# Kernel tuning notes

Measured on AMD Instinct MI355X. Metric: run time of the kernel, lower is better.

The kernel has to match this reference:

```python
import jax, jax.numpy as jnp
import numpy as np

N = 50000   # nodes per graph
E = 500000  # edges per graph
F_IN = 128  # num_features
H = 128     # hidden_channels
C = 64      # num_classes
G = 64      # graphs per batch
NEG_SLOPE = 0.2


def setup_inputs() -> dict:
    key = jax.random.key(0)
    ks = jax.random.split(key, 16)
    s = 1.0 / np.sqrt(H)
    return {
        "x1": jax.random.normal(ks[0], (N, F_IN), jnp.float32),
        "x2": jax.random.normal(ks[1], (N, F_IN), jnp.float32),
        # stacked params for the 2 GATConv layers (F_IN == H so shapes match)
        "convW": jax.random.normal(ks[2], (2, H, H), jnp.float32) * s,
        "att_src": jax.random.normal(ks[3], (2, H), jnp.float32) * s,
        "att_dst": jax.random.normal(ks[4], (2, H), jnp.float32) * s,
        "conv_b": jnp.zeros((2, H), jnp.float32),
        "mlp_w1": jax.random.normal(ks[5], (H, H), jnp.float32) * s,
        "mlp_b1": jnp.zeros((H,), jnp.float32),
        "mlp_w2": jax.random.normal(ks[6], (H, C), jnp.float32) * s,
        "mlp_b2": jnp.zeros((C,), jnp.float32),
        "edge_index1": jax.random.randint(ks[7], (2, E), 0, N, jnp.int64),
        "batch1": jnp.sort(jax.random.randint(ks[8], (N,), 0, G, jnp.int64)),
        "edge_index2": jax.random.randint(ks[9], (2, E), 0, N, jnp.int64),
        "batch2": jnp.sort(jax.random.randint(ks[10], (N,), 0, G, jnp.int64)),
    }


def gat_conv(x, src, dst, W, a_s, a_d, b):
    # PyG GATConv, heads=1, add_self_loops already applied in src/dst
    n = x.shape[0]
    h = x @ W                                   # [N, H]
    alpha_s = h @ a_s                           # [N]
    alpha_d = h @ a_d                           # [N]
    e = alpha_s[src] + alpha_d[dst]             # [Etot]
    e = jnp.where(e > 0, e, NEG_SLOPE * e)      # leaky_relu
    # segment softmax over incoming edges of each dst node
    m = jax.ops.segment_max(e, dst, num_segments=n)
    ex = jnp.exp(e - m[dst])
    denom = jax.ops.segment_sum(ex, dst, num_segments=n)
    alpha = ex / denom[dst]                     # [Etot]
    out = jax.ops.segment_sum(h[src] * alpha[:, None], dst, num_segments=n)
    return out + b


def reference(x1, x2, convW, att_src, att_dst, conv_b,
              mlp_w1, mlp_b1, mlp_w2, mlp_b2,
              edge_index1, batch1, edge_index2, batch2):
    def branch(x, ei):
        n = x.shape[0]
        loops = jnp.arange(n, dtype=ei.dtype)
        src = jnp.concatenate([ei[0], loops])
        dst = jnp.concatenate([ei[1], loops])
        # num_layers=3 -> 2 convs; i != num_layers-1 always true -> ELU after each
        for l in range(2):
            x = gat_conv(x, src, dst, convW[l], att_src[l], att_dst[l], conv_b[l])
            x = jax.nn.elu(x)
            # dropout p=0.5 is identity in eval mode
        return jax.nn.relu(x @ mlp_w1 + mlp_b1) @ mlp_w2 + mlp_b2

    h1 = branch(x1, edge_index1)
    h2 = branch(x2, edge_index2)
    p1 = jax.ops.segment_sum(h1, batch1, num_segments=G)  # [G, C]
    p2 = jax.ops.segment_sum(h2, batch2, num_segments=G)  # [G, C]
    return p1.T @ p2                                      # [C, C]
```

## Files before the change

### kernel.cpp

```cpp
#include <hip/hip_runtime.h>
#include <cstdint>
#include <cstddef>

#define NNODES 50000
#define NEDGES 500000
#define NTOT (NEDGES + NNODES)
#define HDIM 128
#define CDIM 64
#define GDIM 64
#define NB 250
#define NPB 200
#define CHUNK 2048
#define NCHB ((NEDGES + CHUNK - 1) / CHUNK)

typedef __bf16 bf16x8 __attribute__((ext_vector_type(8)));
typedef __bf16 bf16x2 __attribute__((ext_vector_type(2)));
typedef float f32x4 __attribute__((ext_vector_type(4)));


__global__ __launch_bounds__(256) void k_setup(const float* __restrict__ convW,
                                               const float* __restrict__ w1,
                                               const float* __restrict__ w2,
                                               const float* __restrict__ a_s,
                                               const float* __restrict__ a_d,
                                               __bf16* __restrict__ WtC,
                                               __bf16* __restrict__ Wt1,
                                               __bf16* __restrict__ Wt2,
                                               float* __restrict__ Wa,
                                               float* __restrict__ p) {
    int b = blockIdx.x, tid = threadIdx.x;
    if (b < 128) {
        int i = b * 256 + tid;
        int mat = i >> 14, rem = i & 16383;
        int k = rem >> 7, n = rem & 127;
        WtC[mat * 16384 + n * 128 + k] = (__bf16)convW[i];
    } else if (b < 192) {
        int i = (b - 128) * 256 + tid;
        int k = i >> 7, n = i & 127;
        Wt1[n * 128 + k] = (__bf16)w1[i];
    } else if (b < 224) {
        int i = (b - 192) * 256 + tid;
        int k = i >> 6, n = i & 63;
        Wt2[n * 128 + k] = (__bf16)w2[i];
    } else if (b == 224) {
        for (int o = tid; o < 512; o += 256) {
            int l = o >> 8, r = o & 255;
            int type = r >> 7, k = r & 127;
            const float* a = (type ? a_d : a_s) + l * 128;
            const float* Wrow = convW + l * 16384 + k * 128;
            float s = 0.f;
            for (int j = 0; j < 128; j++) s += Wrow[j] * a[j];
            Wa[o] = s;
        }
    } else {
        for (int i = tid; i < 2 * GDIM * CDIM; i += 256) p[i] = 0.f;
    }
}


__global__ __launch_bounds__(256) void k_bhist(const int* __restrict__ ei0,
                                               const int* __restrict__ ei1,
                                               int* __restrict__ bcntB, int e) {
    __shared__ int h[NB];
    const int* dst = (blockIdx.y ? ei1 : ei0) + NEDGES;
    int* bcnt = bcntB + blockIdx.y * NB;
    for (int t = threadIdx.x; t < NB; t += 256) h[t] = 0;
    __syncthreads();
    int base = blockIdx.x * CHUNK;
    int lim = min(base + CHUNK, e);
    for (int i = base + threadIdx.x; i < lim; i += 256) atomicAdd(&h[dst[i] / NPB], 1);
    __syncthreads();
    for (int t = threadIdx.x; t < NB; t += 256)
        if (h[t]) atomicAdd(&bcnt[t], h[t]);
}

__global__ __launch_bounds__(256) void k_bscan(const int* __restrict__ bcntB,
                                               int* __restrict__ boffB,
                                               int* __restrict__ bcurB) {
    __shared__ int s[256];
    int t = threadIdx.x;
    const int* bcnt = bcntB + blockIdx.y * NB;
    int* boff = boffB + blockIdx.y * (NB + 1);
    int* bcur = bcurB + blockIdx.y * NB;
    int v = (t < NB) ? bcnt[t] : 0;
    s[t] = v;
    __syncthreads();
    for (int off = 1; off < 256; off <<= 1) {
        int x = (t >= off) ? s[t - off] : 0;
        __syncthreads();
        s[t] += x;
        __syncthreads();
    }
    if (t < NB) {
        boff[t + 1] = s[t];
        bcur[t] = s[t] - v;
        if (t == 0) boff[0] = 0;
    }
}

__global__ __launch_bounds__(256) void k_part(const int* __restrict__ ei0,
                                              const int* __restrict__ ei1,
                                              int* __restrict__ bcurB,
                                              int2* __restrict__ partB, int e) {
    __shared__ int cnt[NB], boffL[NB], gbase[NB], cur2[NB];
    __shared__ int tmp[256];
    __shared__ int2 staged[CHUNK];
    const int* eis = blockIdx.y ? ei1 : ei0;
    int* bcur = bcurB + blockIdx.y * NB;
    int2* part = partB + blockIdx.y * (size_t)NEDGES;
    int t = threadIdx.x;
    for (int i = t; i < NB; i += 256) { cnt[i] = 0; cur2[i] = 0; }
    __syncthreads();
    int base = blockIdx.x * CHUNK;
    int lim = min(base + CHUNK, e);
    int nloc = lim - base;

    int s_[8], d_[8], b_[8];
    bool v_[8];
#pragma unroll
    for (int k = 0; k < 8; k++) {
        int i = base + k * 256 + t;
        v_[k] = i < lim;
        s_[k] = 0; d_[k] = 0; b_[k] = 0;
        if (v_[k]) {
            s_[k] = eis[i];
            d_[k] = eis[NEDGES + i];
            b_[k] = d_[k] / NPB;
            atomicAdd(&cnt[b_[k]], 1);
        }
    }
    __syncthreads();
    tmp[t] = (t < NB) ? cnt[t] : 0;
    __syncthreads();
    for (int off = 1; off < 256; off <<= 1) {
        int x = (t >= off) ? tmp[t - off] : 0;
        __syncthreads();
        tmp[t] += x;
        __syncthreads();
    }
    if (t < NB) boffL[t] = tmp[t] - cnt[t];
    __syncthreads();
    if (t < NB) {
        int c = cnt[t];
        gbase[t] = c ? atomicAdd(&bcur[t], c) : 0;
    }
    __syncthreads();
#pragma unroll
    for (int k = 0; k < 8; k++) {
        if (v_[k]) {
            int pos = atomicAdd(&cur2[b_[k]], 1);
            staged[boffL[b_[k]] + pos] = make_int2(s_[k], d_[k]);
        }
    }
    __syncthreads();
    for (int i = t; i < nloc; i += 256) {
        int2 r = staged[i];
        int b = r.y / NPB;
        part[gbase[b] + (i - boffL[b])] = r;
    }
}

__global__ __launch_bounds__(256) void k_place(const int2* __restrict__ partB,
                                               const int* __restrict__ boffB,
                                               int* __restrict__ rpB, size_t sNp1,
                                               int* __restrict__ colB, size_t sE) {
    __shared__ int h[NPB];
    __shared__ int lds4[4];
    int b = blockIdx.x;
    const int* boff = boffB + blockIdx.y * (NB + 1);
    const int2* part = partB + blockIdx.y * (size_t)NEDGES;
    int* row_ptr = rpB + blockIdx.y * sNp1;
    int* col = colB + blockIdx.y * sE;
    int t = threadIdx.x;
    int n0 = b * NPB;
    if (t < NPB) h[t] = 0;
    __syncthreads();
    int beg = boff[b], end = boff[b + 1];
    for (int i = beg + t; i < end; i += 256) atomicAdd(&h[part[i].y - n0], 1);
    __syncthreads();
    int v = (t < NPB) ? h[t] : 0;
    int lane = t & 63, wid = t >> 6;
    int incl = v;
#pragma unroll
    for (int off = 1; off < 64; off <<= 1) {
        int nv = __shfl_up(incl, off);
        if (lane >= off) incl += nv;
    }
    if (lane == 63) lds4[wid] = incl;
    __syncthreads();
    if (t == 0) {
        int s = 0;
#pragma unroll
        for (int j = 0; j < 4; j++) { s += lds4[j]; lds4[j] = s; }
    }
    __syncthreads();
    if (wid > 0) incl += lds4[wid - 1];
    if (t < NPB) {
        int rp_end = beg + n0 + incl + t + 1;
        row_ptr[n0 + t + 1] = rp_end;
        int rp_start = rp_end - v - 1;
        col[rp_start] = n0 + t;
        h[t] = rp_start + 1;
        if (b == 0 && t == 0) row_ptr[0] = 0;
    }
    __syncthreads();
    for (int i = beg + t; i < end; i += 256) {
        int2 r = part[i];
        int p = atomicAdd(&h[r.y - n0], 1);
        col[p] = r.x;
    }
}


template <bool AF32>
__global__ __launch_bounds__(256) void k_gemm_conv(const float* __restrict__ x0,
                                                   const float* __restrict__ x1,
                                                   const __bf16* __restrict__ Ab, size_t As_,
                                                   const __bf16* __restrict__ Wt,
                                                   const float* __restrict__ Was,
                                                   const float* __restrict__ Wad,
                                                   float* __restrict__ asB, float* __restrict__ adB,
                                                   size_t aS,
                                                   __bf16* __restrict__ OutB, size_t Os_, int M) {
    constexpr int BN = 128;
    __shared__ __align__(16) unsigned short As[64][136];
    __shared__ __align__(16) unsigned short Bs[BN][136];
    const int tid = threadIdx.x;
    const int lane = tid & 63, w = tid >> 6;
    const int row0 = blockIdx.x * 64;
    __bf16* Out = OutB + blockIdx.y * Os_;

#pragma unroll
    for (int t = 0; t < 4; t++) {
        int ch = t * 256 + tid;
        int r = ch >> 4, cx = ch & 15;
        int grow = row0 + r;
        bf16x8 v = {};
        if (grow < M) {
            if (AF32) {
                const float* Ap = (blockIdx.y ? x1 : x0) + (size_t)grow * 128 + cx * 8;
                float4 f0 = *reinterpret_cast<const float4*>(Ap);
                float4 f1 = *reinterpret_cast<const float4*>(Ap + 4);
                v[0] = (__bf16)f0.x; v[1] = (__bf16)f0.y; v[2] = (__bf16)f0.z; v[3] = (__bf16)f0.w;
                v[4] = (__bf16)f1.x; v[5] = (__bf16)f1.y; v[6] = (__bf16)f1.z; v[7] = (__bf16)f1.w;
            } else {
                v = *reinterpret_cast<const bf16x8*>(Ab + blockIdx.y * As_ + (size_t)grow * 128 + cx * 8);
            }
        }
        *reinterpret_cast<bf16x8*>(&As[r][cx * 8]) = v;
    }
#pragma unroll
    for (int t = 0; t < 8; t++) {
        int ch = t * 256 + tid;
        int r = ch >> 4, cx = ch & 15;
        bf16x8 v = *reinterpret_cast<const bf16x8*>(Wt + (size_t)r * 128 + cx * 8);
        *reinterpret_cast<bf16x8*>(&Bs[r][cx * 8]) = v;
    }
    __syncthreads();

    {
        int row = tid >> 2, seg = tid & 3;
        float ss = 0.f, sd = 0.f;
#pragma unroll
        for (int k = 0; k < 32; k++) {
            int kk = seg * 32 + k;
            float a = __int_as_float(((unsigned)As[row][kk]) << 16);
            ss += a * Was[kk];
            sd += a * Wad[kk];
        }
        ss += __shfl_xor(ss, 1); ss += __shfl_xor(ss, 2);
        sd += __shfl_xor(sd, 1); sd += __shfl_xor(sd, 2);
        if (seg == 0) {
            int grow = row0 + row;
            if (grow < M) {
                (asB + blockIdx.y * aS)[grow] = ss;
                (adB + blockIdx.y * aS)[grow] = sd;
            }
        }
    }

    const int wr0 = (w >> 1) * 32;
    const int wc0 = (w & 1) * 64;
    f32x4 acc[2][4] = {};

#pragma unroll
    for (int ks = 0; ks < 4; ks++) {
        const int koff = ks * 32 + (lane >> 4) * 8;
        bf16x8 af[2], bfr[4];
#pragma unroll
        for (int mf = 0; mf < 2; mf++)
            af[mf] = *reinterpret_cast<const bf16x8*>(&As[wr0 + mf * 16 + (lane & 15)][koff]);
#pragma unroll
        for (int nf = 0; nf < 4; nf++)
            bfr[nf] = *reinterpret_cast<const bf16x8*>(&Bs[wc0 + nf * 16 + (lane & 15)][koff]);
#pragma unroll
        for (int mf = 0; mf < 2; mf++)
#pragma unroll
            for (int nf = 0; nf < 4; nf++)
                acc[mf][nf] = __builtin_amdgcn_mfma_f32_16x16x32_bf16(af[mf], bfr[nf], acc[mf][nf], 0, 0, 0);
    }

#pragma unroll
    for (int mf = 0; mf < 2; mf++) {
#pragma unroll
        for (int r = 0; r < 4; r++) {
            int row = row0 + wr0 + mf * 16 + (lane >> 4) * 4 + r;
            if (row >= M) continue;
#pragma unroll
            for (int nf = 0; nf < 4; nf++) {
                int colc = wc0 + nf * 16 + (lane & 15);
                Out[(size_t)row * BN + colc] = (__bf16)acc[mf][nf][r];
            }
        }
    }
}


__global__ __launch_bounds__(256) void k_gat_agg(const __bf16* __restrict__ hB, size_t hS,
                                                 const float* __restrict__ asB,
                                                 const float* __restrict__ adB, size_t aS,
                                                 const int* __restrict__ rpB, size_t sNp1,
                                                 const int* __restrict__ colB, size_t sE,
                                                 const float* __restrict__ bias,
                                                 __bf16* __restrict__ outB, size_t oS, int n) {
    int grp = threadIdx.x >> 4;
    int node = blockIdx.x * 16 + grp;
    int l = threadIdx.x & 15;
    if (node >= n) return;
    const float* alpha_s = asB + blockIdx.y * aS;
    const int* row_ptr = rpB + blockIdx.y * sNp1;
    const int* col = colB + blockIdx.y * sE;
    const char* hbase = (const char*)(hB + blockIdx.y * hS);
    float ad = (adB + blockIdx.y * aS)[node];
    int beg = row_ptr[node], end = row_ptr[node + 1];
    int deg = end - beg;
    int foff = l * 16;

    float acc[8] = {0.f, 0.f, 0.f, 0.f, 0.f, 0.f, 0.f, 0.f};

    if (deg <= 16) {
        bool v = l < deg;
        int c = 0;
        float e = -1e30f;
        if (v) {
            c = col[beg + l];
            float t = alpha_s[c] + ad;
            e = (t > 0.f) ? t : 0.2f * t;
        }
        float m = e;
#pragma unroll
        for (int off = 8; off; off >>= 1) m = fmaxf(m, __shfl_xor(m, off));
        float ex = v ? __expf(e - m) : 0.f;
        float den = ex;
#pragma unroll
        for (int off = 8; off; off >>= 1) den += __shfl_xor(den, off);
        float wn = ex / den;

        int base = (grp << 4) & 63;
        for (int e2 = 0; e2 < deg; e2 += 2) {
            int i1 = base + e2, i2 = base + e2 + 1;
            int s1 = __shfl(c, i1); float w1 = __shfl(wn, i1);
            int s2 = __shfl(c, i2); float w2 = __shfl(wn, i2);
            bool h2v = (e2 + 1) < deg;
            s2 = h2v ? s2 : s1;
            w2 = h2v ? w2 : 0.f;
            bf16x8 h1 = *reinterpret_cast<const bf16x8*>(hbase + ((size_t)(unsigned)s1 << 8) + foff);
            bf16x8 hh2 = *reinterpret_cast<const bf16x8*>(hbase + ((size_t)(unsigned)s2 << 8) + foff);
#pragma unroll
            for (int q = 0; q < 8; q++) acc[q] += w1 * (float)h1[q] + w2 * (float)hh2[q];
        }
    } else {
        float m = -1e30f;
        for (int i = beg + l; i < end; i += 16) {
            float t = alpha_s[col[i]] + ad;
            t = (t > 0.f) ? t : 0.2f * t;
            m = fmaxf(m, t);
        }
#pragma unroll
        for (int off = 8; off; off >>= 1) m = fmaxf(m, __shfl_xor(m, off));
        float den = 0.f;
        for (int i = beg + l; i < end; i += 16) {
            float t = alpha_s[col[i]] + ad;
            t = (t > 0.f) ? t : 0.2f * t;
            den += __expf(t - m);
        }
#pragma unroll
        for (int off = 8; off; off >>= 1) den += __shfl_xor(den, off);
        float rinv = 1.f / den;
        for (int e2 = beg; e2 < end; e2++) {
            int cc = col[e2];
            float t = alpha_s[cc] + ad;
            t = (t > 0.f) ? t : 0.2f * t;
            float wv = __expf(t - m) * rinv;
            bf16x8 hv = *reinterpret_cast<const bf16x8*>(hbase + ((size_t)(unsigned)cc << 8) + foff);
#pragma unroll
            for (int q = 0; q < 8; q++) acc[q] += wv * (float)hv[q];
        }
    }

    float4 b0 = *reinterpret_cast<const float4*>(bias + l * 8);
    float4 b1 = *reinterpret_cast<const float4*>(bias + l * 8 + 4);
    float bb[8] = {b0.x, b0.y, b0.z, b0.w, b1.x, b1.y, b1.z, b1.w};
    bf16x8 o;
#pragma unroll
    for (int q = 0; q < 8; q++) {
        float x = acc[q] + bb[q];
        x = (x > 0.f) ? x : __expf(x) - 1.f;
        o[q] = (__bf16)x;
    }
    *reinterpret_cast<bf16x8*>((char*)(outB + blockIdx.y * oS) + ((size_t)(unsigned)node << 8) + foff) = o;
}


__global__ __launch_bounds__(256) void k_mlp_pool(const __bf16* __restrict__ AbB, size_t As_,
                                                  const __bf16* __restrict__ Wt1,
                                                  const __bf16* __restrict__ Wt2,
                                                  const float* __restrict__ b1,
                                                  const float* __restrict__ b2,
                                                  const int* __restrict__ bat0,
                                                  const int* __restrict__ bat1,
                                                  float* __restrict__ pB, size_t pS, int M) {
    __shared__ __align__(16) unsigned short As[64][136];
    __shared__ __align__(16) unsigned short Bs[128][136];
    const int tid = threadIdx.x;
    const int lane = tid & 63, w = tid >> 6;
    const int row0 = blockIdx.x * 64;
    const __bf16* Ab = AbB + blockIdx.y * As_;
    const int* batch = blockIdx.y ? bat1 : bat0;
    float* p = pB + blockIdx.y * pS;

#pragma unroll
    for (int t = 0; t < 4; t++) {
        int ch = t * 256 + tid;
        int r = ch >> 4, cx = ch & 15;
        int grow = row0 + r;
        bf16x8 v = {};
        if (grow < M) v = *reinterpret_cast<const bf16x8*>(Ab + (size_t)grow * 128 + cx * 8);
        *reinterpret_cast<bf16x8*>(&As[r][cx * 8]) = v;
    }
#pragma unroll
    for (int t = 0; t < 8; t++) {
        int ch = t * 256 + tid;
        int r = ch >> 4, cx = ch & 15;
        bf16x8 v = *reinterpret_cast<const bf16x8*>(Wt1 + (size_t)r * 128 + cx * 8);
        *reinterpret_cast<bf16x8*>(&Bs[r][cx * 8]) = v;
    }
    __syncthreads();

    {
        const int wr0 = (w >> 1) * 32;
        const int wc0 = (w & 1) * 64;
        f32x4 acc[2][4] = {};
#pragma unroll
        for (int ks = 0; ks < 4; ks++) {
            const int koff = ks * 32 + (lane >> 4) * 8;
            bf16x8 af[2], bfr[4];
#pragma unroll
            for (int mf = 0; mf < 2; mf++)
                af[mf] = *reinterpret_cast<const bf16x8*>(&As[wr0 + mf * 16 + (lane & 15)][koff]);
#pragma unroll
            for (int nf = 0; nf < 4; nf++)
                bfr[nf] = *reinterpret_cast<const bf16x8*>(&Bs[wc0 + nf * 16 + (lane & 15)][koff]);
#pragma unroll
            for (int mf = 0; mf < 2; mf++)
#pragma unroll
                for (int nf = 0; nf < 4; nf++)
                    acc[mf][nf] = __builtin_amdgcn_mfma_f32_16x16x32_bf16(af[mf], bfr[nf], acc[mf][nf], 0, 0, 0);
        }
        __syncthreads();
#pragma unroll
        for (int mf = 0; mf < 2; mf++)
#pragma unroll
            for (int r = 0; r < 4; r++) {
                int row = wr0 + mf * 16 + (lane >> 4) * 4 + r;
#pragma unroll
                for (int nf = 0; nf < 4; nf++) {
                    int colc = wc0 + nf * 16 + (lane & 15);
                    float v = fmaxf(acc[mf][nf][r] + b1[colc], 0.f);
                    As[row][colc] = __builtin_bit_cast(unsigned short, (__bf16)v);
                }
            }
#pragma unroll
        for (int t = 0; t < 4; t++) {
            int ch = t * 256 + tid;
            int r = ch >> 4, cx = ch & 15;
            bf16x8 v = *reinterpret_cast<const bf16x8*>(Wt2 + (size_t)r * 128 + cx * 8);
            *reinterpret_cast<bf16x8*>(&Bs[r][cx * 8]) = v;
        }
        __syncthreads();
    }

    const int wr2 = w * 16;
    f32x4 acc2[4] = {};
#pragma unroll
    for (int ks = 0; ks < 4; ks++) {
        const int koff = ks * 32 + (lane >> 4) * 8;
        bf16x8 a2 = *reinterpret_cast<const bf16x8*>(&As[wr2 + (lane & 15)][koff]);
#pragma unroll
        for (int nf = 0; nf < 4; nf++) {
            bf16x8 bf2 = *reinterpret_cast<const bf16x8*>(&Bs[nf * 16 + (lane & 15)][koff]);
            acc2[nf] = __builtin_amdgcn_mfma_f32_16x16x32_bf16(a2, bf2, acc2[nf], 0, 0, 0);
        }
    }

    int q = lane >> 4, c = lane & 15;
    bool full = (row0 + 63) < M;
    int g0 = batch[min(row0, M - 1)];
    int g1 = batch[min(row0 + 63, M - 1)];
    if (full && g0 == g1) {
        float s0 = acc2[0][0] + acc2[0][1] + acc2[0][2] + acc2[0][3];
        float s1 = acc2[1][0] + acc2[1][1] + acc2[1][2] + acc2[1][3];
        float s2 = acc2[2][0] + acc2[2][1] + acc2[2][2] + acc2[2][3];
        float s3 = acc2[3][0] + acc2[3][1] + acc2[3][2] + acc2[3][3];
        s0 += __shfl_xor(s0, 16); s0 += __shfl_xor(s0, 32);
        s1 += __shfl_xor(s1, 16); s1 += __shfl_xor(s1, 32);
        s2 += __shfl_xor(s2, 16); s2 += __shfl_xor(s2, 32);
        s3 += __shfl_xor(s3, 16); s3 += __shfl_xor(s3, 32);
        float v = (q & 2) ? ((q & 1) ? s3 : s2) : ((q & 1) ? s1 : s0);
        v += 16.f * b2[q * 16 + c];
        atomicAdd(&p[g0 * CDIM + q * 16 + c], v);
    } else {
        float b2v[4];
#pragma unroll
        for (int nf = 0; nf < 4; nf++) b2v[nf] = b2[nf * 16 + c];
#pragma unroll
        for (int r = 0; r < 4; r++) {
            int row = row0 + wr2 + q * 4 + r;
            if (row >= M) continue;
            int g = batch[row];
#pragma unroll
            for (int nf = 0; nf < 4; nf++)
                atomicAdd(&p[g * CDIM + nf * 16 + c], acc2[nf][r] + b2v[nf]);
        }
    }
}


__global__ __launch_bounds__(64) void k_final(const float* __restrict__ p, float* __restrict__ out) {
    int i = blockIdx.x;
    int j = threadIdx.x;
    const float* p1 = p;
    const float* p2 = p + GDIM * CDIM;
    float s = 0.f;
    for (int g = 0; g < GDIM; ++g) s += p1[g * CDIM + i] * p2[g * CDIM + j];
    out[i * CDIM + j] = s;
}


static inline size_t align_up(size_t x, size_t a) { return (x + a - 1) & ~(a - 1); }

struct Ws {
    __bf16 *Hb, *Yb;
    __bf16 *WtC, *Wt1, *Wt2;
    float *alpha_s, *alpha_d, *Wa, *p;
    int *row_ptr, *col;
    int *bcnt, *boff, *bcur;
    int2* part;
    size_t sNH, sN, sNp1, sE;
    size_t need;
};

static Ws carve(void* ws, bool combined) {
    char* p = (char*)ws;
    size_t off = 0;
    Ws w;
    int nb = combined ? 2 : 1;
    auto take = [&](size_t bytes) {
        char* r = p + off;
        off = align_up(off + bytes, 256);
        return r;
    };
    w.Hb = (__bf16*)take((size_t)nb * NNODES * HDIM * 2);
    w.Yb = (__bf16*)take((size_t)nb * NNODES * HDIM * 2);
    w.alpha_s = (float*)take((size_t)nb * NNODES * 4);
    w.alpha_d = (float*)take((size_t)nb * NNODES * 4);
    w.col = (int*)take((size_t)nb * NTOT * 4);
    w.part = (int2*)take((size_t)nb * NEDGES * 8);
    w.row_ptr = (int*)take((size_t)nb * (NNODES + 1) * 4);
    w.bcnt = (int*)take((size_t)2 * NB * 4);
    w.boff = (int*)take((size_t)2 * (NB + 1) * 4);
    w.bcur = (int*)take((size_t)2 * NB * 4);
    w.WtC = (__bf16*)take((size_t)2 * HDIM * HDIM * 2);
    w.Wt1 = (__bf16*)take((size_t)HDIM * HDIM * 2);
    w.Wt2 = (__bf16*)take((size_t)HDIM * CDIM * 2);
    w.Wa = (float*)take((size_t)512 * 4);
    w.p = (float*)take((size_t)2 * GDIM * CDIM * 4);
    w.need = off;
    size_t s = combined ? 1 : 0;
    w.sNH = s * (size_t)NNODES * HDIM;
    w.sN = s * (size_t)NNODES;
    w.sNp1 = s * (size_t)(NNODES + 1);
    w.sE = s * (size_t)NTOT;
    return w;
}

static void pipeline(const Ws& w, const float* xA, const float* xB,
                     const int* eiA, const int* eiB,
                     const int* batA, const int* batB,
                     const float* conv_b, const float* b1, const float* b2,
                     float* pbase, size_t pstride, int yc, hipStream_t stream) {
    const int N = NNODES, E = NEDGES;
    dim3 gC(NCHB, yc), gB(NB, yc), g1(1, yc);
    dim3 gW((N + 15) / 16, yc);
    dim3 gG((N + 63) / 64, yc);

    hipMemsetAsync(w.bcnt, 0, (size_t)yc * NB * 4, stream);
    k_bhist<<<gC, 256, 0, stream>>>(eiA, eiB, w.bcnt, E);
    k_bscan<<<g1, 256, 0, stream>>>(w.bcnt, w.boff, w.bcur);
    k_part<<<gC, 256, 0, stream>>>(eiA, eiB, w.bcur, w.part, E);
    k_place<<<gB, 256, 0, stream>>>(w.part, w.boff, w.row_ptr, w.sNp1, w.col, w.sE);

    k_gemm_conv<true><<<gG, 256, 0, stream>>>(
        xA, xB, nullptr, 0, w.WtC, w.Wa, w.Wa + 128,
        w.alpha_s, w.alpha_d, w.sN, w.Hb, w.sNH, N);
    k_gat_agg<<<gW, 256, 0, stream>>>(w.Hb, w.sNH, w.alpha_s, w.alpha_d, w.sN,
                                      w.row_ptr, w.sNp1, w.col, w.sE, conv_b, w.Yb, w.sNH, N);
    k_gemm_conv<false><<<gG, 256, 0, stream>>>(
        nullptr, nullptr, w.Yb, w.sNH, w.WtC + HDIM * HDIM, w.Wa + 256, w.Wa + 384,
        w.alpha_s, w.alpha_d, w.sN, w.Hb, w.sNH, N);
    k_gat_agg<<<gW, 256, 0, stream>>>(w.Hb, w.sNH, w.alpha_s, w.alpha_d, w.sN,
                                      w.row_ptr, w.sNp1, w.col, w.sE, conv_b + HDIM, w.Yb, w.sNH, N);
    k_mlp_pool<<<gG, 256, 0, stream>>>(w.Yb, w.sNH, w.Wt1, w.Wt2, b1, b2,
                                       batA, batB, pbase, pstride, N);
}

extern "C" void kernel_launch(void* const* d_in, const int* in_sizes, int n_in, void* d_out,
                              int out_size, void* d_ws, size_t ws_size, hipStream_t stream) {
    const float* x1      = (const float*)d_in[0];
    const float* x2      = (const float*)d_in[1];
    const float* convW   = (const float*)d_in[2];
    const float* att_src = (const float*)d_in[3];
    const float* att_dst = (const float*)d_in[4];
    const float* conv_b  = (const float*)d_in[5];
    const float* mlp_w1  = (const float*)d_in[6];
    const float* mlp_b1  = (const float*)d_in[7];
    const float* mlp_w2  = (const float*)d_in[8];
    const float* mlp_b2  = (const float*)d_in[9];
    const int* ei1       = (const int*)d_in[10];
    const int* batch1    = (const int*)d_in[11];
    const int* ei2       = (const int*)d_in[12];
    const int* batch2    = (const int*)d_in[13];
    float* out = (float*)d_out;

    Ws wc = carve(d_ws, true);
    bool combined = ws_size >= wc.need;
    Ws w = combined ? wc : carve(d_ws, false);

    k_setup<<<226, 256, 0, stream>>>(convW, mlp_w1, mlp_w2, att_src, att_dst,
                                     w.WtC, w.Wt1, w.Wt2, w.Wa, w.p);

    if (combined) {
        pipeline(w, x1, x2, ei1, ei2, batch1, batch2, conv_b,
                 mlp_b1, mlp_b2, w.p, (size_t)GDIM * CDIM, 2, stream);
    } else {
        pipeline(w, x1, x1, ei1, ei1, batch1, batch1, conv_b,
                 mlp_b1, mlp_b2, w.p, 0, 1, stream);
        pipeline(w, x2, x2, ei2, ei2, batch2, batch2, conv_b,
                 mlp_b1, mlp_b2, w.p + GDIM * CDIM, 0, 1, stream);
    }

    k_final<<<CDIM, 64, 0, stream>>>(w.p, out);
}
```

Before: 346.9 us.

## Pack partitioned edges into 32-bit words and batch neighbor gathers eight-wide

The edge partition buffer now stores each edge as one 32-bit word holding the source id, the local destination and the bucket. This halves the traffic written by k_part and read by k_place. In the GAT aggregation kernel, a new gather16 helper broadcasts up to 16 neighbor indices and weights through shuffles and issues eight row loads before accumulating, so more memory requests are in flight. The high-degree path now computes column indices and softmax weights across lanes instead of serially per edge. The packing assumes node ids fit in 16 bits and per-bucket offsets fit in 8 bits, which holds for the fixed sizes.

```diff
diff --git a/kernel.cpp b/kernel.cpp
--- a/kernel.cpp
+++ b/kernel.cpp
@@ -101,13 +101,13 @@
 __global__ __launch_bounds__(256) void k_part(const int* __restrict__ ei0,
                                               const int* __restrict__ ei1,
                                               int* __restrict__ bcurB,
-                                              int2* __restrict__ partB, int e) {
+                                              unsigned int* __restrict__ partB, int e) {
     __shared__ int cnt[NB], boffL[NB], gbase[NB], cur2[NB];
     __shared__ int tmp[256];
-    __shared__ int2 staged[CHUNK];
+    __shared__ unsigned int staged[CHUNK];
     const int* eis = blockIdx.y ? ei1 : ei0;
     int* bcur = bcurB + blockIdx.y * NB;
-    int2* part = partB + blockIdx.y * (size_t)NEDGES;
+    unsigned int* part = partB + blockIdx.y * (size_t)NEDGES;
     int t = threadIdx.x;
     for (int i = t; i < NB; i += 256) { cnt[i] = 0; cur2[i] = 0; }
     __syncthreads();
@@ -115,17 +115,20 @@
     int lim = min(base + CHUNK, e);
     int nloc = lim - base;
 
-    int s_[8], d_[8], b_[8];
+    int s_[8], b_[8];
+    unsigned int pk_[8];
     bool v_[8];
 #pragma unroll
     for (int k = 0; k < 8; k++) {
         int i = base + k * 256 + t;
         v_[k] = i < lim;
-        s_[k] = 0; d_[k] = 0; b_[k] = 0;
+        pk_[k] = 0; b_[k] = 0;
         if (v_[k]) {
             s_[k] = eis[i];
-            d_[k] = eis[NEDGES + i];
-            b_[k] = d_[k] / NPB;
+            int d = eis[NEDGES + i];
+            b_[k] = d / NPB;
+            int dloc = d - b_[k] * NPB;
+            pk_[k] = (unsigned)s_[k] | ((unsigned)dloc << 16) | ((unsigned)b_[k] << 24);
             atomicAdd(&cnt[b_[k]], 1);
         }
     }
@@ -149,18 +152,18 @@
     for (int k = 0; k < 8; k++) {
         if (v_[k]) {
             int pos = atomicAdd(&cur2[b_[k]], 1);
-            staged[boffL[b_[k]] + pos] = make_int2(s_[k], d_[k]);
+            staged[boffL[b_[k]] + pos] = pk_[k];
         }
     }
     __syncthreads();
     for (int i = t; i < nloc; i += 256) {
-        int2 r = staged[i];
-        int b = r.y / NPB;
+        unsigned int r = staged[i];
+        int b = (int)(r >> 24);
         part[gbase[b] + (i - boffL[b])] = r;
     }
 }
 
-__global__ __launch_bounds__(256) void k_place(const int2* __restrict__ partB,
+__global__ __launch_bounds__(256) void k_place(const unsigned int* __restrict__ partB,
                                                const int* __restrict__ boffB,
                                                int* __restrict__ rpB, size_t sNp1,
                                                int* __restrict__ colB, size_t sE) {
@@ -168,7 +171,7 @@
     __shared__ int lds4[4];
     int b = blockIdx.x;
     const int* boff = boffB + blockIdx.y * (NB + 1);
-    const int2* part = partB + blockIdx.y * (size_t)NEDGES;
+    const unsigned int* part = partB + blockIdx.y * (size_t)NEDGES;
     int* row_ptr = rpB + blockIdx.y * sNp1;
     int* col = colB + blockIdx.y * sE;
     int t = threadIdx.x;
@@ -176,7 +179,7 @@
     if (t < NPB) h[t] = 0;
     __syncthreads();
     int beg = boff[b], end = boff[b + 1];
-    for (int i = beg + t; i < end; i += 256) atomicAdd(&h[part[i].y - n0], 1);
+    for (int i = beg + t; i < end; i += 256) atomicAdd(&h[(part[i] >> 16) & 0xFF], 1);
     __syncthreads();
     int v = (t < NPB) ? h[t] : 0;
     int lane = t & 63, wid = t >> 6;
@@ -205,9 +208,9 @@
     }
     __syncthreads();
     for (int i = beg + t; i < end; i += 256) {
-        int2 r = part[i];
-        int p = atomicAdd(&h[r.y - n0], 1);
-        col[p] = r.x;
+        unsigned int r = part[i];
+        int p = atomicAdd(&h[(r >> 16) & 0xFF], 1);
+        col[p] = (int)(r & 0xFFFF);
     }
 }
 
@@ -315,6 +318,30 @@
     }
 }
 
+
+__device__ __forceinline__ void gather16(const char* __restrict__ hbase, int foff, int base,
+                                         int c, float wn, int cnt, float (&acc)[8]) {
+#pragma unroll
+    for (int j0 = 0; j0 < 16; j0 += 8) {
+        if (j0 < cnt) {
+            bf16x8 hv[8];
+            float ww[8];
+#pragma unroll
+            for (int j = 0; j < 8; j++) {
+                int cj = __shfl(c, base + j0 + j);
+                float wj = __shfl(wn, base + j0 + j);
+                bool lv = (j0 + j) < cnt;
+                ww[j] = lv ? wj : 0.f;
+                const char* ap = hbase + ((size_t)(unsigned)cj << 8) + foff;
+                hv[j] = lv ? *reinterpret_cast<const bf16x8*>(ap) : bf16x8{};
+            }
+#pragma unroll
+            for (int j = 0; j < 8; j++)
+#pragma unroll
+                for (int q = 0; q < 8; q++) acc[q] += ww[j] * (float)hv[j][q];
+        }
+    }
+}
 
 __global__ __launch_bounds__(256) void k_gat_agg(const __bf16* __restrict__ hB, size_t hS,
                                                  const float* __restrict__ asB,
@@ -335,6 +362,7 @@
     int beg = row_ptr[node], end = row_ptr[node + 1];
     int deg = end - beg;
     int foff = l * 16;
+    int base = (threadIdx.x & 63) & 48;
 
     float acc[8] = {0.f, 0.f, 0.f, 0.f, 0.f, 0.f, 0.f, 0.f};
 
@@ -355,20 +383,7 @@
 #pragma unroll
         for (int off = 8; off; off >>= 1) den += __shfl_xor(den, off);
         float wn = ex / den;
-
-        int base = (grp << 4) & 63;
-        for (int e2 = 0; e2 < deg; e2 += 2) {
-            int i1 = base + e2, i2 = base + e2 + 1;
-            int s1 = __shfl(c, i1); float w1 = __shfl(wn, i1);
-            int s2 = __shfl(c, i2); float w2 = __shfl(wn, i2);
-            bool h2v = (e2 + 1) < deg;
-            s2 = h2v ? s2 : s1;
-            w2 = h2v ? w2 : 0.f;
-            bf16x8 h1 = *reinterpret_cast<const bf16x8*>(hbase + ((size_t)(unsigned)s1 << 8) + foff);
-            bf16x8 hh2 = *reinterpret_cast<const bf16x8*>(hbase + ((size_t)(unsigned)s2 << 8) + foff);
-#pragma unroll
-            for (int q = 0; q < 8; q++) acc[q] += w1 * (float)h1[q] + w2 * (float)hh2[q];
-        }
+        gather16(hbase, foff, base, c, wn, deg, acc);
     } else {
         float m = -1e30f;
         for (int i = beg + l; i < end; i += 16) {
@@ -387,14 +402,18 @@
 #pragma unroll
         for (int off = 8; off; off >>= 1) den += __shfl_xor(den, off);
         float rinv = 1.f / den;
-        for (int e2 = beg; e2 < end; e2++) {
-            int cc = col[e2];
-            float t = alpha_s[cc] + ad;
-            t = (t > 0.f) ? t : 0.2f * t;
-            float wv = __expf(t - m) * rinv;
-            bf16x8 hv = *reinterpret_cast<const bf16x8*>(hbase + ((size_t)(unsigned)cc << 8) + foff);
-#pragma unroll
-            for (int q = 0; q < 8; q++) acc[q] += wv * (float)hv[q];
+        for (int i0 = beg; i0 < end; i0 += 16) {
+            int idx = i0 + l;
+            bool lv = idx < end;
+            int cb = lv ? col[idx] : 0;
+            float wv = 0.f;
+            if (lv) {
+                float t = alpha_s[cb] + ad;
+                t = (t > 0.f) ? t : 0.2f * t;
+                wv = __expf(t - m) * rinv;
+            }
+            int cnt = min(end - i0, 16);
+            gather16(hbase, foff, base, cb, wv, cnt, acc);
         }
     }
 
@@ -555,7 +574,7 @@
     float *alpha_s, *alpha_d, *Wa, *p;
     int *row_ptr, *col;
     int *bcnt, *boff, *bcur;
-    int2* part;
+    unsigned int* part;
     size_t sNH, sN, sNp1, sE;
     size_t need;
 };
@@ -575,7 +594,7 @@
     w.alpha_s = (float*)take((size_t)nb * NNODES * 4);
     w.alpha_d = (float*)take((size_t)nb * NNODES * 4);
     w.col = (int*)take((size_t)nb * NTOT * 4);
-    w.part = (int2*)take((size_t)nb * NEDGES * 8);
+    w.part = (unsigned int*)take((size_t)nb * NEDGES * 4);
     w.row_ptr = (int*)take((size_t)nb * (NNODES + 1) * 4);
     w.bcnt = (int*)take((size_t)2 * NB * 4);
     w.boff = (int*)take((size_t)2 * (NB + 1) * 4);
```

Result: no change. 351.0 us (+1.2%).
